# Optimization experiments

Hardware: AMD Instinct MI355X
Metric: run time of the kernel (lower is better)

## Reference

```python
import jax, jax.numpy as jnp
import numpy as np

N_NODES = 10000
N_EDGES = 320000
NEG_SLOPE = 0.2  # PyG GATConv default leaky_relu slope
EPS = 1e-16      # PyG softmax denominator epsilon


def setup_inputs() -> dict:
    key = jax.random.key(0)
    ks = jax.random.split(key, 9)
    x = jax.random.normal(ks[0], (N_NODES, 128), dtype=jnp.float32)
    edge_index = jax.random.randint(ks[1], (2, N_EDGES), 0, N_NODES, dtype=jnp.int64)
    W1 = jax.random.normal(ks[2], (128, 320), dtype=jnp.float32) * 0.05
    att_src1 = jax.random.normal(ks[3], (5, 64), dtype=jnp.float32) * 0.1
    att_dst1 = jax.random.normal(ks[4], (5, 64), dtype=jnp.float32) * 0.1
    b1 = jnp.zeros((320,), dtype=jnp.float32)
    W2 = jax.random.normal(ks[5], (320, 64), dtype=jnp.float32) * 0.05
    att_src2 = jax.random.normal(ks[6], (1, 64), dtype=jnp.float32) * 0.1
    att_dst2 = jax.random.normal(ks[7], (1, 64), dtype=jnp.float32) * 0.1
    b2 = jnp.zeros((64,), dtype=jnp.float32)
    return {"x": x, "edge_index": edge_index, "W1": W1, "att_src1": att_src1,
            "att_dst1": att_dst1, "b1": b1, "W2": W2, "att_src2": att_src2,
            "att_dst2": att_dst2, "b2": b2}


def gat_conv(x, src, dst, W, att_src, att_dst, bias, heads, out_c, concat):
    """PyG-style GATConv (eval mode, self-loops already in src/dst)."""
    N = x.shape[0]
    h = (x @ W).reshape(N, heads, out_c)                 # [N, H, C]
    a_src = jnp.einsum('nhc,hc->nh', h, att_src)         # [N, H]
    a_dst = jnp.einsum('nhc,hc->nh', h, att_dst)         # [N, H]
    e = a_src[src] + a_dst[dst]                          # [E, H]
    e = jax.nn.leaky_relu(e, NEG_SLOPE)
    # segment softmax over incoming edges of each destination node
    m = jax.ops.segment_max(e, dst, num_segments=N)      # [N, H]
    ex = jnp.exp(e - m[dst])
    s = jax.ops.segment_sum(ex, dst, num_segments=N)     # [N, H]
    alpha = ex / (s[dst] + EPS)                          # [E, H]
    out = jax.ops.segment_sum(h[src] * alpha[:, :, None], dst, num_segments=N)
    if concat:
        out = out.reshape(N, heads * out_c)
    else:
        out = out.mean(axis=1)
    return out + bias


def reference(x, edge_index, W1, att_src1, att_dst1, b1, W2, att_src2, att_dst2, b2):
    N = x.shape[0]
    loop = jnp.arange(N, dtype=edge_index.dtype)
    src = jnp.concatenate([edge_index[0], loop])  # add self-loops (PyG default)
    dst = jnp.concatenate([edge_index[1], loop])
    h = jax.nn.relu(gat_conv(x, src, dst, W1, att_src1, att_dst1, b1, 5, 64, True))
    h = jax.nn.relu(gat_conv(h, src, dst, W2, att_src2, att_dst2, b2, 1, 64, False))
    # F.dropout with training=False is identity (eval mode)
    return h
```

## Files before the change

kernel.cpp:

```cpp
#include <hip/hip_runtime.h>
#include <hip/hip_fp16.h>
#include <math.h>

#define N_NODES 10000
#define N_EDGES 320000
#define ET (N_EDGES + N_NODES)
#define CAP 128
#define NB_G1 (157 * 5)
#define NB_SCT ((ET + 255) / 256)

__device__ __forceinline__ float lrelu_exp(float e) {
  e = (e > 0.f) ? e : 0.2f * e;
  return __expf(e);
}

__device__ __forceinline__ void ld_half8(const __half* p, float4& lo, float4& hi) {
  uint4 u = *reinterpret_cast<const uint4*>(p);
  float2 f0 = __half22float2(*reinterpret_cast<const __half2*>(&u.x));
  float2 f1 = __half22float2(*reinterpret_cast<const __half2*>(&u.y));
  float2 f2 = __half22float2(*reinterpret_cast<const __half2*>(&u.z));
  float2 f3 = __half22float2(*reinterpret_cast<const __half2*>(&u.w));
  lo = make_float4(f0.x, f0.y, f1.x, f1.y);
  hi = make_float4(f2.x, f2.y, f3.x, f3.y);
}

__device__ __forceinline__ void st_half4(__half* p, float4 v) {
  __half2 lo = __float22half2_rn(make_float2(v.x, v.y));
  __half2 hi = __float22half2_rn(make_float2(v.z, v.w));
  uint2 u;
  u.x = *reinterpret_cast<const unsigned*>(&lo);
  u.y = *reinterpret_cast<const unsigned*>(&hi);
  *reinterpret_cast<uint2*>(p) = u;
}


__global__ __launch_bounds__(256) void k_init(int* __restrict__ cursor) {
  int i = blockIdx.x * 256 + threadIdx.x;
  if (i < N_NODES) cursor[i] = 0;
}


__global__ __launch_bounds__(256) void k_gemm1_scatter(const float* __restrict__ x, const float* __restrict__ W1,
                                                       const float* __restrict__ att_src, const float* __restrict__ att_dst,
                                                       __half* __restrict__ h1, float* __restrict__ a_src,
                                                       float* __restrict__ a_dst,
                                                       const int* __restrict__ ei, int* __restrict__ cursor,
                                                       int* __restrict__ csr) {
  __shared__ float xs[128][65];
  int bid = blockIdx.x;
  int t = threadIdx.x;
  if (bid >= NB_G1) {
    int i = (bid - NB_G1) * 256 + t;
    if (i < ET) {
      int src, dst;
      if (i < N_EDGES) { src = ei[i]; dst = ei[N_EDGES + i]; }
      else             { src = dst = i - N_EDGES; }
      int pos = (dst << 7) + atomicAdd(&cursor[dst], 1);
      csr[pos] = src;
    }
    return;
  }
  int h = bid / 157;
  int rb = (bid % 157) * 64;
#pragma unroll
  for (int i = 0; i < 8; ++i) {
    int idx = t + 256 * i;
    int kq = (idx & 31) * 4;
    int row = idx >> 5;
    int gr = rb + row;
    float4 v = make_float4(0.f, 0.f, 0.f, 0.f);
    if (gr < N_NODES) v = *reinterpret_cast<const float4*>(&x[(size_t)gr * 128 + kq]);
    xs[kq + 0][row] = v.x; xs[kq + 1][row] = v.y; xs[kq + 2][row] = v.z; xs[kq + 3][row] = v.w;
  }
  __syncthreads();
  int cg = t & 15, rg = t >> 4;
  int c0 = cg * 4, r0 = rg * 4;
  const float* __restrict__ wp = W1 + h * 64 + c0;
  float4 a0 = make_float4(0.f,0.f,0.f,0.f), a1 = a0, a2 = a0, a3 = a0;
#pragma unroll 4
  for (int k = 0; k < 128; ++k) {
    float4 xv = *reinterpret_cast<const float4*>(&xs[k][r0]);
    float4 wv = *reinterpret_cast<const float4*>(&wp[(size_t)k * 320]);
    a0.x = fmaf(xv.x, wv.x, a0.x); a0.y = fmaf(xv.x, wv.y, a0.y); a0.z = fmaf(xv.x, wv.z, a0.z); a0.w = fmaf(xv.x, wv.w, a0.w);
    a1.x = fmaf(xv.y, wv.x, a1.x); a1.y = fmaf(xv.y, wv.y, a1.y); a1.z = fmaf(xv.y, wv.z, a1.z); a1.w = fmaf(xv.y, wv.w, a1.w);
    a2.x = fmaf(xv.z, wv.x, a2.x); a2.y = fmaf(xv.z, wv.y, a2.y); a2.z = fmaf(xv.z, wv.z, a2.z); a2.w = fmaf(xv.z, wv.w, a2.w);
    a3.x = fmaf(xv.w, wv.x, a3.x); a3.y = fmaf(xv.w, wv.y, a3.y); a3.z = fmaf(xv.w, wv.z, a3.z); a3.w = fmaf(xv.w, wv.w, a3.w);
  }
  float4 asv = *reinterpret_cast<const float4*>(&att_src[h * 64 + c0]);
  float4 adv = *reinterpret_cast<const float4*>(&att_dst[h * 64 + c0]);
#pragma unroll
  for (int rr = 0; rr < 4; ++rr) {
    float4 ar = (rr == 0) ? a0 : (rr == 1) ? a1 : (rr == 2) ? a2 : a3;
    float vs = ar.x * asv.x + ar.y * asv.y + ar.z * asv.z + ar.w * asv.w;
    float vd = ar.x * adv.x + ar.y * adv.y + ar.z * adv.z + ar.w * adv.w;
#pragma unroll
    for (int m = 1; m < 16; m <<= 1) { vs += __shfl_xor(vs, m); vd += __shfl_xor(vd, m); }
    int gr = rb + r0 + rr;
    if (gr < N_NODES) {
      if (cg == 0) { a_src[h * N_NODES + gr] = vs; a_dst[h * N_NODES + gr] = vd; }
      st_half4(&h1[(size_t)gr * 320 + h * 64 + c0], ar);
    }
  }
}


__global__ __launch_bounds__(256) void k_agg1(const __half* __restrict__ h1, const float* __restrict__ a_src,
                                              const float* __restrict__ a_dst, const float* __restrict__ b1,
                                              const int* __restrict__ degs, const int* __restrict__ csr,
                                              float* __restrict__ out1) {
  int lane = threadIdx.x & 63, wid = threadIdx.x >> 6;
  int n = blockIdx.x * 4 + wid;
  int h = blockIdx.y;
  int sub = lane >> 3;
  int cg = lane & 7;
  int beg = n << 7;
  int deg = degs[n];
  int limit = beg + deg;
  int end = beg + ((deg + 15) & ~15);
  const float* __restrict__ as = a_src + (size_t)h * N_NODES;
  float adn = a_dst[(size_t)h * N_NODES + n];
  const __half* __restrict__ hh = h1 + h * 64 + cg * 8;
  float4 aclo = make_float4(0.f, 0.f, 0.f, 0.f), achi = aclo;
  float s = 0.f;
  int e = beg + sub;
  bool va = e < limit, vb = e + 8 < limit;
  int t0 = csr[e], t1 = csr[e + 8];
  unsigned i0 = va ? (unsigned)t0 : 0u, i1 = vb ? (unsigned)t1 : 0u;
  float v0 = as[i0], v1 = as[i1];
  for (;;) {
    float4 galo, gahi, gblo, gbhi;
    ld_half8(hh + i0 * 320u, galo, gahi);
    ld_half8(hh + i1 * 320u, gblo, gbhi);
    float pa = va ? lrelu_exp(v0 + adn) : 0.f;
    float pb = vb ? lrelu_exp(v1 + adn) : 0.f;
    e += 16;
    bool more = e < end;
    if (more) {
      va = e < limit; vb = e + 8 < limit;
      t0 = csr[e]; t1 = csr[e + 8];
      i0 = va ? (unsigned)t0 : 0u; i1 = vb ? (unsigned)t1 : 0u;
      v0 = as[i0]; v1 = as[i1];
    }
    s += pa + pb;
    aclo.x = fmaf(pb, gblo.x, fmaf(pa, galo.x, aclo.x));
    aclo.y = fmaf(pb, gblo.y, fmaf(pa, galo.y, aclo.y));
    aclo.z = fmaf(pb, gblo.z, fmaf(pa, galo.z, aclo.z));
    aclo.w = fmaf(pb, gblo.w, fmaf(pa, galo.w, aclo.w));
    achi.x = fmaf(pb, gbhi.x, fmaf(pa, gahi.x, achi.x));
    achi.y = fmaf(pb, gbhi.y, fmaf(pa, gahi.y, achi.y));
    achi.z = fmaf(pb, gbhi.z, fmaf(pa, gahi.z, achi.z));
    achi.w = fmaf(pb, gbhi.w, fmaf(pa, gahi.w, achi.w));
    if (!more) break;
  }
#pragma unroll
  for (int m = 8; m <= 32; m <<= 1) {
    aclo.x += __shfl_xor(aclo.x, m);
    aclo.y += __shfl_xor(aclo.y, m);
    aclo.z += __shfl_xor(aclo.z, m);
    aclo.w += __shfl_xor(aclo.w, m);
    achi.x += __shfl_xor(achi.x, m);
    achi.y += __shfl_xor(achi.y, m);
    achi.z += __shfl_xor(achi.z, m);
    achi.w += __shfl_xor(achi.w, m);
    s += __shfl_xor(s, m);
  }
  if (sub == 0) {
    float inv = 1.f / (s + 1e-16f);
    const float* bp = b1 + h * 64 + cg * 8;
    float4 b_lo = *reinterpret_cast<const float4*>(bp);
    float4 b_hi = *reinterpret_cast<const float4*>(bp + 4);
    float4 olo, ohi;
    olo.x = fmaxf(fmaf(aclo.x, inv, b_lo.x), 0.f);
    olo.y = fmaxf(fmaf(aclo.y, inv, b_lo.y), 0.f);
    olo.z = fmaxf(fmaf(aclo.z, inv, b_lo.z), 0.f);
    olo.w = fmaxf(fmaf(aclo.w, inv, b_lo.w), 0.f);
    ohi.x = fmaxf(fmaf(achi.x, inv, b_hi.x), 0.f);
    ohi.y = fmaxf(fmaf(achi.y, inv, b_hi.y), 0.f);
    ohi.z = fmaxf(fmaf(achi.z, inv, b_hi.z), 0.f);
    ohi.w = fmaxf(fmaf(achi.w, inv, b_hi.w), 0.f);
    float* op = &out1[(size_t)n * 320 + h * 64 + cg * 8];
    *reinterpret_cast<float4*>(op) = olo;
    *reinterpret_cast<float4*>(op + 4) = ohi;
  }
}

__global__ __launch_bounds__(256) void k_agg2(const __half* __restrict__ h2, const float* __restrict__ a_src,
                                              const float* __restrict__ a_dst, const float* __restrict__ b2,
                                              const int* __restrict__ degs, const int* __restrict__ csr,
                                              float* __restrict__ out) {
  int lane = threadIdx.x & 63, wid = threadIdx.x >> 6;
  int n = blockIdx.x * 4 + wid;
  int sub = lane >> 3;
  int cg = lane & 7;
  int beg = n << 7;
  int deg = degs[n];
  int limit = beg + deg;
  int end = beg + ((deg + 15) & ~15);
  float adn = a_dst[n];
  const __half* __restrict__ hh = h2 + cg * 8;
  float4 aclo = make_float4(0.f, 0.f, 0.f, 0.f), achi = aclo;
  float s = 0.f;
  int e = beg + sub;
  bool va = e < limit, vb = e + 8 < limit;
  int t0 = csr[e], t1 = csr[e + 8];
  unsigned i0 = va ? (unsigned)t0 : 0u, i1 = vb ? (unsigned)t1 : 0u;
  float v0 = a_src[i0], v1 = a_src[i1];
  for (;;) {
    float4 galo, gahi, gblo, gbhi;
    ld_half8(hh + i0 * 64u, galo, gahi);
    ld_half8(hh + i1 * 64u, gblo, gbhi);
    float pa = va ? lrelu_exp(v0 + adn) : 0.f;
    float pb = vb ? lrelu_exp(v1 + adn) : 0.f;
    e += 16;
    bool more = e < end;
    if (more) {
      va = e < limit; vb = e + 8 < limit;
      t0 = csr[e]; t1 = csr[e + 8];
      i0 = va ? (unsigned)t0 : 0u; i1 = vb ? (unsigned)t1 : 0u;
      v0 = a_src[i0]; v1 = a_src[i1];
    }
    s += pa + pb;
    aclo.x = fmaf(pb, gblo.x, fmaf(pa, galo.x, aclo.x));
    aclo.y = fmaf(pb, gblo.y, fmaf(pa, galo.y, aclo.y));
    aclo.z = fmaf(pb, gblo.z, fmaf(pa, galo.z, aclo.z));
    aclo.w = fmaf(pb, gblo.w, fmaf(pa, galo.w, aclo.w));
    achi.x = fmaf(pb, gbhi.x, fmaf(pa, gahi.x, achi.x));
    achi.y = fmaf(pb, gbhi.y, fmaf(pa, gahi.y, achi.y));
    achi.z = fmaf(pb, gbhi.z, fmaf(pa, gahi.z, achi.z));
    achi.w = fmaf(pb, gbhi.w, fmaf(pa, gahi.w, achi.w));
    if (!more) break;
  }
#pragma unroll
  for (int m = 8; m <= 32; m <<= 1) {
    aclo.x += __shfl_xor(aclo.x, m);
    aclo.y += __shfl_xor(aclo.y, m);
    aclo.z += __shfl_xor(aclo.z, m);
    aclo.w += __shfl_xor(aclo.w, m);
    achi.x += __shfl_xor(achi.x, m);
    achi.y += __shfl_xor(achi.y, m);
    achi.z += __shfl_xor(achi.z, m);
    achi.w += __shfl_xor(achi.w, m);
    s += __shfl_xor(s, m);
  }
  if (sub == 0) {
    float inv = 1.f / (s + 1e-16f);
    const float* bp = b2 + cg * 8;
    float4 b_lo = *reinterpret_cast<const float4*>(bp);
    float4 b_hi = *reinterpret_cast<const float4*>(bp + 4);
    float4 olo, ohi;
    olo.x = fmaxf(fmaf(aclo.x, inv, b_lo.x), 0.f);
    olo.y = fmaxf(fmaf(aclo.y, inv, b_lo.y), 0.f);
    olo.z = fmaxf(fmaf(aclo.z, inv, b_lo.z), 0.f);
    olo.w = fmaxf(fmaf(aclo.w, inv, b_lo.w), 0.f);
    ohi.x = fmaxf(fmaf(achi.x, inv, b_hi.x), 0.f);
    ohi.y = fmaxf(fmaf(achi.y, inv, b_hi.y), 0.f);
    ohi.z = fmaxf(fmaf(achi.z, inv, b_hi.z), 0.f);
    ohi.w = fmaxf(fmaf(achi.w, inv, b_hi.w), 0.f);
    float* op = &out[(size_t)n * 64 + cg * 8];
    *reinterpret_cast<float4*>(op) = olo;
    *reinterpret_cast<float4*>(op + 4) = ohi;
  }
}


__global__ __launch_bounds__(256) void k_gemm2(const float* __restrict__ out1, const float* __restrict__ W2,
                                               float* __restrict__ h2part) {
  __shared__ float xs[64][65];
  int t = threadIdx.x;
  int rb = blockIdx.x * 64;
  int kc = blockIdx.y;
#pragma unroll
  for (int i = 0; i < 4; ++i) {
    int idx = t + 256 * i;
    int kq = (idx & 15) * 4;
    int row = idx >> 4;
    int gr = rb + row;
    float4 v = make_float4(0.f, 0.f, 0.f, 0.f);
    if (gr < N_NODES) v = *reinterpret_cast<const float4*>(&out1[(size_t)gr * 320 + kc * 64 + kq]);
    xs[kq + 0][row] = v.x; xs[kq + 1][row] = v.y; xs[kq + 2][row] = v.z; xs[kq + 3][row] = v.w;
  }
  __syncthreads();
  int cg = t & 15, rg = t >> 4;
  int c0 = cg * 4, r0 = rg * 4;
  const float* __restrict__ wp = W2 + (size_t)kc * 64 * 64 + c0;
  float4 a0 = make_float4(0.f,0.f,0.f,0.f), a1 = a0, a2 = a0, a3 = a0;
#pragma unroll 4
  for (int k = 0; k < 64; ++k) {
    float4 xv = *reinterpret_cast<const float4*>(&xs[k][r0]);
    float4 wv = *reinterpret_cast<const float4*>(&wp[(size_t)k * 64]);
    a0.x = fmaf(xv.x, wv.x, a0.x); a0.y = fmaf(xv.x, wv.y, a0.y); a0.z = fmaf(xv.x, wv.z, a0.z); a0.w = fmaf(xv.x, wv.w, a0.w);
    a1.x = fmaf(xv.y, wv.x, a1.x); a1.y = fmaf(xv.y, wv.y, a1.y); a1.z = fmaf(xv.y, wv.z, a1.z); a1.w = fmaf(xv.y, wv.w, a1.w);
    a2.x = fmaf(xv.z, wv.x, a2.x); a2.y = fmaf(xv.z, wv.y, a2.y); a2.z = fmaf(xv.z, wv.z, a2.z); a2.w = fmaf(xv.z, wv.w, a2.w);
    a3.x = fmaf(xv.w, wv.x, a3.x); a3.y = fmaf(xv.w, wv.y, a3.y); a3.z = fmaf(xv.w, wv.z, a3.z); a3.w = fmaf(xv.w, wv.w, a3.w);
  }
  float* __restrict__ hp = h2part + (size_t)kc * N_NODES * 64;
#pragma unroll
  for (int rr = 0; rr < 4; ++rr) {
    float4 ar = (rr == 0) ? a0 : (rr == 1) ? a1 : (rr == 2) ? a2 : a3;
    int gr = rb + r0 + rr;
    if (gr < N_NODES) *reinterpret_cast<float4*>(&hp[(size_t)gr * 64 + c0]) = ar;
  }
}


__global__ __launch_bounds__(256) void k_hred2(const float* __restrict__ h2part,
                                               const float* __restrict__ att_src, const float* __restrict__ att_dst,
                                               __half* __restrict__ h2, float* __restrict__ a_src,
                                               float* __restrict__ a_dst) {
  int n = blockIdx.x * 4 + (threadIdx.x >> 6);
  int c = threadIdx.x & 63;
  if (n >= N_NODES) return;
  float v = 0.f;
#pragma unroll
  for (int kc = 0; kc < 5; ++kc) v += h2part[((size_t)kc * N_NODES + n) * 64 + c];
  float vs = v * att_src[c], vd = v * att_dst[c];
  float vnext = __shfl_down(v, 1);
  if ((c & 1) == 0) {
    __half2 p = __float22half2_rn(make_float2(v, vnext));
    *reinterpret_cast<unsigned*>(&h2[(size_t)n * 64 + c]) = *reinterpret_cast<const unsigned*>(&p);
  }
  for (int off = 32; off; off >>= 1) {
    vs += __shfl_down(vs, off);
    vd += __shfl_down(vd, off);
  }
  if (c == 0) { a_src[n] = vs; a_dst[n] = vd; }
}


extern "C" void kernel_launch(void* const* d_in, const int* in_sizes, int n_in,
                              void* d_out, int out_size, void* d_ws, size_t ws_size,
                              hipStream_t stream) {
  (void)in_sizes; (void)n_in; (void)out_size; (void)ws_size;
  const float* x    = (const float*)d_in[0];
  const int*   ei   = (const int*)d_in[1];
  const float* W1   = (const float*)d_in[2];
  const float* as1w = (const float*)d_in[3];
  const float* ad1w = (const float*)d_in[4];
  const float* b1   = (const float*)d_in[5];
  const float* W2   = (const float*)d_in[6];
  const float* as2w = (const float*)d_in[7];
  const float* ad2w = (const float*)d_in[8];
  const float* b2   = (const float*)d_in[9];
  float* out = (float*)d_out;

  char* ws = (char*)d_ws;
  size_t off = 0;
  auto alloc = [&](size_t bytes) -> void* {
    void* p = ws + off;
    off += (bytes + 255) & ~(size_t)255;
    return p;
  };
  __half* h1     = (__half*)alloc((size_t)N_NODES * 320 * 2);
  float*  out1   = (float*)alloc((size_t)N_NODES * 320 * 4);
  __half* h2     = (__half*)alloc((size_t)N_NODES * 64 * 2);
  float*  h2part = (float*)alloc((size_t)5 * N_NODES * 64 * 4);
  float*  a_src1 = (float*)alloc((size_t)5 * N_NODES * 4);
  float*  a_dst1 = (float*)alloc((size_t)5 * N_NODES * 4);
  float*  a_src2 = (float*)alloc((size_t)N_NODES * 4);
  float*  a_dst2 = (float*)alloc((size_t)N_NODES * 4);
  int*    cursor = (int*)alloc((size_t)N_NODES * 4);
  int*    csr    = (int*)alloc((size_t)N_NODES * CAP * 4);

  k_init<<<(N_NODES + 255) / 256, 256, 0, stream>>>(cursor);
  k_gemm1_scatter<<<NB_G1 + NB_SCT, 256, 0, stream>>>(x, W1, as1w, ad1w, h1, a_src1, a_dst1,
                                                      ei, cursor, csr);
  {
    dim3 g(N_NODES / 4, 5);
    k_agg1 <<<g, 256, 0, stream>>>(h1, a_src1, a_dst1, b1, cursor, csr, out1);
  }
  {
    dim3 g((N_NODES + 63) / 64, 5);
    k_gemm2<<<g, 256, 0, stream>>>(out1, W2, h2part);
  }
  k_hred2<<<(N_NODES + 3) / 4, 256, 0, stream>>>(h2part, as2w, ad2w, h2, a_src2, a_dst2);
  k_agg2 <<<N_NODES / 4, 256, 0, stream>>>(h2, a_src2, a_dst2, b2, cursor, csr, out);
}
```

Measured before the change: 96.77 us.

## Run both GEMMs in fp16 with packed dot2 and fp16 intermediates

```diff
diff --git a/kernel.cpp b/kernel.cpp
--- a/kernel.cpp
+++ b/kernel.cpp
@@ -1,6 +1,10 @@
 #include <hip/hip_runtime.h>
 #include <hip/hip_fp16.h>
 #include <math.h>
+
+#ifndef __has_builtin
+#define __has_builtin(x) 0
+#endif
 
 #define N_NODES 10000
 #define N_EDGES 320000
@@ -8,6 +12,32 @@
 #define CAP 128
 #define NB_G1 (157 * 5)
 #define NB_SCT ((ET + 255) / 256)
+
+#define IB_CUR 40
+#define IB_X   1250
+#define IB_W1  160
+#define IB_W2  80
+#define NB_INIT (IB_CUR + IB_X + IB_W1 + IB_W2)
+
+typedef _Float16 f16x2 __attribute__((ext_vector_type(2)));
+
+__device__ __forceinline__ float dot2f(unsigned xu, unsigned wu, float acc) {
+  f16x2 xv = *reinterpret_cast<const f16x2*>(&xu);
+  f16x2 wv = *reinterpret_cast<const f16x2*>(&wu);
+#if __has_builtin(__builtin_amdgcn_fdot2)
+  return __builtin_amdgcn_fdot2(xv, wv, acc, false);
+#else
+  return acc + (float)xv.x * (float)wv.x + (float)xv.y * (float)wv.y;
+#endif
+}
+
+__device__ __forceinline__ float dot8(uint4 x, uint4 w, float acc) {
+  acc = dot2f(x.x, w.x, acc);
+  acc = dot2f(x.y, w.y, acc);
+  acc = dot2f(x.z, w.z, acc);
+  acc = dot2f(x.w, w.w, acc);
+  return acc;
+}
 
 __device__ __forceinline__ float lrelu_exp(float e) {
   e = (e > 0.f) ? e : 0.2f * e;
@@ -33,20 +63,57 @@
   *reinterpret_cast<uint2*>(p) = u;
 }
 
-
-__global__ __launch_bounds__(256) void k_init(int* __restrict__ cursor) {
-  int i = blockIdx.x * 256 + threadIdx.x;
-  if (i < N_NODES) cursor[i] = 0;
-}
-
-
-__global__ __launch_bounds__(256) void k_gemm1_scatter(const float* __restrict__ x, const float* __restrict__ W1,
+__device__ __forceinline__ void st_half8(__half* p, float4 lo, float4 hi) {
+  __half2 q0 = __float22half2_rn(make_float2(lo.x, lo.y));
+  __half2 q1 = __float22half2_rn(make_float2(lo.z, lo.w));
+  __half2 q2 = __float22half2_rn(make_float2(hi.x, hi.y));
+  __half2 q3 = __float22half2_rn(make_float2(hi.z, hi.w));
+  uint4 u;
+  u.x = *reinterpret_cast<const unsigned*>(&q0);
+  u.y = *reinterpret_cast<const unsigned*>(&q1);
+  u.z = *reinterpret_cast<const unsigned*>(&q2);
+  u.w = *reinterpret_cast<const unsigned*>(&q3);
+  *reinterpret_cast<uint4*>(p) = u;
+}
+
+
+__global__ __launch_bounds__(256) void k_init(int* __restrict__ cursor,
+                                              const float* __restrict__ x, __half* __restrict__ xh,
+                                              const float* __restrict__ W1, __half* __restrict__ W1t,
+                                              const float* __restrict__ W2, __half* __restrict__ W2t) {
+  int bid = blockIdx.x, t = threadIdx.x;
+  if (bid < IB_CUR) {
+    int i = bid * 256 + t;
+    if (i < N_NODES) cursor[i] = 0;
+  } else if (bid < IB_CUR + IB_X) {
+    int idx = (bid - IB_CUR) * 256 + t;
+    if (idx < N_NODES * 32) {
+      float4 v = *reinterpret_cast<const float4*>(&x[(size_t)idx * 4]);
+      st_half4(&xh[(size_t)idx * 4], v);
+    }
+  } else if (bid < IB_CUR + IB_X + IB_W1) {
+    int idx = (bid - IB_CUR - IB_X) * 256 + t;
+    if (idx < 128 * 320) {
+      int k = idx / 320, c = idx % 320;
+      W1t[(size_t)c * 128 + k] = __float2half_rn(W1[idx]);
+    }
+  } else {
+    int idx = (bid - IB_CUR - IB_X - IB_W1) * 256 + t;
+    if (idx < 320 * 64) {
+      int k = idx / 64, c = idx % 64;
+      W2t[(size_t)c * 320 + k] = __float2half_rn(W2[idx]);
+    }
+  }
+}
+
+
+__global__ __launch_bounds__(256) void k_gemm1_scatter(const __half* __restrict__ xh, const __half* __restrict__ W1t,
                                                        const float* __restrict__ att_src, const float* __restrict__ att_dst,
                                                        __half* __restrict__ h1, float* __restrict__ a_src,
                                                        float* __restrict__ a_dst,
                                                        const int* __restrict__ ei, int* __restrict__ cursor,
                                                        int* __restrict__ csr) {
-  __shared__ float xs[128][65];
+  __shared__ __half xs_h[64][136];
   int bid = blockIdx.x;
   int t = threadIdx.x;
   if (bid >= NB_G1) {
@@ -63,28 +130,33 @@
   int h = bid / 157;
   int rb = (bid % 157) * 64;
 #pragma unroll
-  for (int i = 0; i < 8; ++i) {
+  for (int i = 0; i < 4; ++i) {
     int idx = t + 256 * i;
-    int kq = (idx & 31) * 4;
-    int row = idx >> 5;
+    int row = idx >> 4, ko = idx & 15;
     int gr = rb + row;
-    float4 v = make_float4(0.f, 0.f, 0.f, 0.f);
-    if (gr < N_NODES) v = *reinterpret_cast<const float4*>(&x[(size_t)gr * 128 + kq]);
-    xs[kq + 0][row] = v.x; xs[kq + 1][row] = v.y; xs[kq + 2][row] = v.z; xs[kq + 3][row] = v.w;
+    uint4 v = make_uint4(0, 0, 0, 0);
+    if (gr < N_NODES) v = *reinterpret_cast<const uint4*>(&xh[(size_t)gr * 128 + ko * 8]);
+    *reinterpret_cast<uint4*>(&xs_h[row][ko * 8]) = v;
   }
   __syncthreads();
   int cg = t & 15, rg = t >> 4;
   int c0 = cg * 4, r0 = rg * 4;
-  const float* __restrict__ wp = W1 + h * 64 + c0;
-  float4 a0 = make_float4(0.f,0.f,0.f,0.f), a1 = a0, a2 = a0, a3 = a0;
+  const __half* __restrict__ wt = W1t + (size_t)(h * 64 + c0) * 128;
+  float4 a0 = make_float4(0.f, 0.f, 0.f, 0.f), a1 = a0, a2 = a0, a3 = a0;
 #pragma unroll 4
-  for (int k = 0; k < 128; ++k) {
-    float4 xv = *reinterpret_cast<const float4*>(&xs[k][r0]);
-    float4 wv = *reinterpret_cast<const float4*>(&wp[(size_t)k * 320]);
-    a0.x = fmaf(xv.x, wv.x, a0.x); a0.y = fmaf(xv.x, wv.y, a0.y); a0.z = fmaf(xv.x, wv.z, a0.z); a0.w = fmaf(xv.x, wv.w, a0.w);
-    a1.x = fmaf(xv.y, wv.x, a1.x); a1.y = fmaf(xv.y, wv.y, a1.y); a1.z = fmaf(xv.y, wv.z, a1.z); a1.w = fmaf(xv.y, wv.w, a1.w);
-    a2.x = fmaf(xv.z, wv.x, a2.x); a2.y = fmaf(xv.z, wv.y, a2.y); a2.z = fmaf(xv.z, wv.z, a2.z); a2.w = fmaf(xv.z, wv.w, a2.w);
-    a3.x = fmaf(xv.w, wv.x, a3.x); a3.y = fmaf(xv.w, wv.y, a3.y); a3.z = fmaf(xv.w, wv.z, a3.z); a3.w = fmaf(xv.w, wv.w, a3.w);
+  for (int ko = 0; ko < 16; ++ko) {
+    uint4 x0 = *reinterpret_cast<const uint4*>(&xs_h[r0 + 0][ko * 8]);
+    uint4 x1 = *reinterpret_cast<const uint4*>(&xs_h[r0 + 1][ko * 8]);
+    uint4 x2 = *reinterpret_cast<const uint4*>(&xs_h[r0 + 2][ko * 8]);
+    uint4 x3 = *reinterpret_cast<const uint4*>(&xs_h[r0 + 3][ko * 8]);
+    uint4 w0 = *reinterpret_cast<const uint4*>(wt + 0 * 128 + ko * 8);
+    uint4 w1 = *reinterpret_cast<const uint4*>(wt + 1 * 128 + ko * 8);
+    uint4 w2 = *reinterpret_cast<const uint4*>(wt + 2 * 128 + ko * 8);
+    uint4 w3 = *reinterpret_cast<const uint4*>(wt + 3 * 128 + ko * 8);
+    a0.x = dot8(x0, w0, a0.x); a0.y = dot8(x0, w1, a0.y); a0.z = dot8(x0, w2, a0.z); a0.w = dot8(x0, w3, a0.w);
+    a1.x = dot8(x1, w0, a1.x); a1.y = dot8(x1, w1, a1.y); a1.z = dot8(x1, w2, a1.z); a1.w = dot8(x1, w3, a1.w);
+    a2.x = dot8(x2, w0, a2.x); a2.y = dot8(x2, w1, a2.y); a2.z = dot8(x2, w2, a2.z); a2.w = dot8(x2, w3, a2.w);
+    a3.x = dot8(x3, w0, a3.x); a3.y = dot8(x3, w1, a3.y); a3.z = dot8(x3, w2, a3.z); a3.w = dot8(x3, w3, a3.w);
   }
   float4 asv = *reinterpret_cast<const float4*>(&att_src[h * 64 + c0]);
   float4 adv = *reinterpret_cast<const float4*>(&att_dst[h * 64 + c0]);
@@ -107,7 +179,7 @@
 __global__ __launch_bounds__(256) void k_agg1(const __half* __restrict__ h1, const float* __restrict__ a_src,
                                               const float* __restrict__ a_dst, const float* __restrict__ b1,
                                               const int* __restrict__ degs, const int* __restrict__ csr,
-                                              float* __restrict__ out1) {
+                                              __half* __restrict__ out1h) {
   int lane = threadIdx.x & 63, wid = threadIdx.x >> 6;
   int n = blockIdx.x * 4 + wid;
   int h = blockIdx.y;
@@ -178,9 +250,7 @@
     ohi.y = fmaxf(fmaf(achi.y, inv, b_hi.y), 0.f);
     ohi.z = fmaxf(fmaf(achi.z, inv, b_hi.z), 0.f);
     ohi.w = fmaxf(fmaf(achi.w, inv, b_hi.w), 0.f);
-    float* op = &out1[(size_t)n * 320 + h * 64 + cg * 8];
-    *reinterpret_cast<float4*>(op) = olo;
-    *reinterpret_cast<float4*>(op + 4) = ohi;
+    st_half8(&out1h[(size_t)n * 320 + h * 64 + cg * 8], olo, ohi);
   }
 }
 
@@ -263,35 +333,40 @@
 }
 
 
-__global__ __launch_bounds__(256) void k_gemm2(const float* __restrict__ out1, const float* __restrict__ W2,
+__global__ __launch_bounds__(256) void k_gemm2(const __half* __restrict__ out1h, const __half* __restrict__ W2t,
                                                float* __restrict__ h2part) {
-  __shared__ float xs[64][65];
+  __shared__ __half xs_h[64][72];
   int t = threadIdx.x;
   int rb = blockIdx.x * 64;
   int kc = blockIdx.y;
 #pragma unroll
-  for (int i = 0; i < 4; ++i) {
+  for (int i = 0; i < 2; ++i) {
     int idx = t + 256 * i;
-    int kq = (idx & 15) * 4;
-    int row = idx >> 4;
+    int row = idx >> 3, ko = idx & 7;
     int gr = rb + row;
-    float4 v = make_float4(0.f, 0.f, 0.f, 0.f);
-    if (gr < N_NODES) v = *reinterpret_cast<const float4*>(&out1[(size_t)gr * 320 + kc * 64 + kq]);
-    xs[kq + 0][row] = v.x; xs[kq + 1][row] = v.y; xs[kq + 2][row] = v.z; xs[kq + 3][row] = v.w;
+    uint4 v = make_uint4(0, 0, 0, 0);
+    if (gr < N_NODES) v = *reinterpret_cast<const uint4*>(&out1h[(size_t)gr * 320 + kc * 64 + ko * 8]);
+    *reinterpret_cast<uint4*>(&xs_h[row][ko * 8]) = v;
   }
   __syncthreads();
   int cg = t & 15, rg = t >> 4;
   int c0 = cg * 4, r0 = rg * 4;
-  const float* __restrict__ wp = W2 + (size_t)kc * 64 * 64 + c0;
-  float4 a0 = make_float4(0.f,0.f,0.f,0.f), a1 = a0, a2 = a0, a3 = a0;
-#pragma unroll 4
-  for (int k = 0; k < 64; ++k) {
-    float4 xv = *reinterpret_cast<const float4*>(&xs[k][r0]);
-    float4 wv = *reinterpret_cast<const float4*>(&wp[(size_t)k * 64]);
-    a0.x = fmaf(xv.x, wv.x, a0.x); a0.y = fmaf(xv.x, wv.y, a0.y); a0.z = fmaf(xv.x, wv.z, a0.z); a0.w = fmaf(xv.x, wv.w, a0.w);
-    a1.x = fmaf(xv.y, wv.x, a1.x); a1.y = fmaf(xv.y, wv.y, a1.y); a1.z = fmaf(xv.y, wv.z, a1.z); a1.w = fmaf(xv.y, wv.w, a1.w);
-    a2.x = fmaf(xv.z, wv.x, a2.x); a2.y = fmaf(xv.z, wv.y, a2.y); a2.z = fmaf(xv.z, wv.z, a2.z); a2.w = fmaf(xv.z, wv.w, a2.w);
-    a3.x = fmaf(xv.w, wv.x, a3.x); a3.y = fmaf(xv.w, wv.y, a3.y); a3.z = fmaf(xv.w, wv.z, a3.z); a3.w = fmaf(xv.w, wv.w, a3.w);
+  const __half* __restrict__ wt = W2t + (size_t)c0 * 320 + kc * 64;
+  float4 a0 = make_float4(0.f, 0.f, 0.f, 0.f), a1 = a0, a2 = a0, a3 = a0;
+#pragma unroll
+  for (int ko = 0; ko < 8; ++ko) {
+    uint4 x0 = *reinterpret_cast<const uint4*>(&xs_h[r0 + 0][ko * 8]);
+    uint4 x1 = *reinterpret_cast<const uint4*>(&xs_h[r0 + 1][ko * 8]);
+    uint4 x2 = *reinterpret_cast<const uint4*>(&xs_h[r0 + 2][ko * 8]);
+    uint4 x3 = *reinterpret_cast<const uint4*>(&xs_h[r0 + 3][ko * 8]);
+    uint4 w0 = *reinterpret_cast<const uint4*>(wt + 0 * 320 + ko * 8);
+    uint4 w1 = *reinterpret_cast<const uint4*>(wt + 1 * 320 + ko * 8);
+    uint4 w2 = *reinterpret_cast<const uint4*>(wt + 2 * 320 + ko * 8);
+    uint4 w3 = *reinterpret_cast<const uint4*>(wt + 3 * 320 + ko * 8);
+    a0.x = dot8(x0, w0, a0.x); a0.y = dot8(x0, w1, a0.y); a0.z = dot8(x0, w2, a0.z); a0.w = dot8(x0, w3, a0.w);
+    a1.x = dot8(x1, w0, a1.x); a1.y = dot8(x1, w1, a1.y); a1.z = dot8(x1, w2, a1.z); a1.w = dot8(x1, w3, a1.w);
+    a2.x = dot8(x2, w0, a2.x); a2.y = dot8(x2, w1, a2.y); a2.z = dot8(x2, w2, a2.z); a2.w = dot8(x2, w3, a2.w);
+    a3.x = dot8(x3, w0, a3.x); a3.y = dot8(x3, w1, a3.y); a3.z = dot8(x3, w2, a3.z); a3.w = dot8(x3, w3, a3.w);
   }
   float* __restrict__ hp = h2part + (size_t)kc * N_NODES * 64;
 #pragma unroll
@@ -350,8 +425,11 @@
     off += (bytes + 255) & ~(size_t)255;
     return p;
   };
+  __half* xh     = (__half*)alloc((size_t)N_NODES * 128 * 2);
+  __half* W1t    = (__half*)alloc((size_t)320 * 128 * 2);
+  __half* W2t    = (__half*)alloc((size_t)64 * 320 * 2);
   __half* h1     = (__half*)alloc((size_t)N_NODES * 320 * 2);
-  float*  out1   = (float*)alloc((size_t)N_NODES * 320 * 4);
+  __half* out1h  = (__half*)alloc((size_t)N_NODES * 320 * 2);
   __half* h2     = (__half*)alloc((size_t)N_NODES * 64 * 2);
   float*  h2part = (float*)alloc((size_t)5 * N_NODES * 64 * 4);
   float*  a_src1 = (float*)alloc((size_t)5 * N_NODES * 4);
@@ -361,16 +439,16 @@
   int*    cursor = (int*)alloc((size_t)N_NODES * 4);
   int*    csr    = (int*)alloc((size_t)N_NODES * CAP * 4);
 
-  k_init<<<(N_NODES + 255) / 256, 256, 0, stream>>>(cursor);
-  k_gemm1_scatter<<<NB_G1 + NB_SCT, 256, 0, stream>>>(x, W1, as1w, ad1w, h1, a_src1, a_dst1,
+  k_init<<<NB_INIT, 256, 0, stream>>>(cursor, x, xh, W1, W1t, W2, W2t);
+  k_gemm1_scatter<<<NB_G1 + NB_SCT, 256, 0, stream>>>(xh, W1t, as1w, ad1w, h1, a_src1, a_dst1,
                                                       ei, cursor, csr);
   {
     dim3 g(N_NODES / 4, 5);
-    k_agg1 <<<g, 256, 0, stream>>>(h1, a_src1, a_dst1, b1, cursor, csr, out1);
+    k_agg1 <<<g, 256, 0, stream>>>(h1, a_src1, a_dst1, b1, cursor, csr, out1h);
   }
   {
     dim3 g((N_NODES + 63) / 64, 5);
-    k_gemm2<<<g, 256, 0, stream>>>(out1, W2, h2part);
+    k_gemm2<<<g, 256, 0, stream>>>(out1h, W2t, h2part);
   }
   k_hred2<<<(N_NODES + 3) / 4, 256, 0, stream>>>(h2part, as2w, ad2w, h2, a_src2, a_dst2);
   k_agg2 <<<N_NODES / 4, 256, 0, stream>>>(h2, a_src2, a_dst2, b2, cursor, csr, out);
```

Result: slower. 122.4 us (+26.5%).
